# Kernel optimization log

Hardware: AMD Instinct MI355X
Metric: run time of the kernel (lower is better)

## Reference

```python
import jax
jax.config.update("jax_enable_x64", True)
import jax.numpy as jnp
import numpy as np

B = 4            # batch size
Z, Y, X = 41, 1024, 1024   # spatial shape (all coords < 1025, matching the hash base)
NT = 2_000_000   # raw teacher voxels (with duplicates)
NS = 800_000     # student voxels (subset of teacher unique coords)
C = 32           # feature channels
M = 1025         # hash base from the original module


def _hash(idx):
    # idx: [N,4] int -> int64 scalar hash; batch in high bits so sorting the hash
    # == lexicographic sort by (batch, c1, c2, c3), matching torch.unique(dim=0).
    w = jnp.array([M ** 3, M ** 2, M, 1], dtype=jnp.int64)
    return idx.astype(jnp.int64) @ w


def setup_inputs() -> dict:
    rng = np.random.default_rng(0)
    b = rng.integers(0, B, NT)
    z = rng.integers(0, Z, NT)
    y = rng.integers(0, Y, NT)
    x = rng.integers(0, X, NT)
    teacher_indices = np.stack([b, z, y, x], axis=1).astype(np.int32)

    # student indices must be a subset of teacher's unique coords (forward asserts this)
    h = (b.astype(np.int64) * M ** 3 + z.astype(np.int64) * M ** 2
         + y.astype(np.int64) * M + x.astype(np.int64))
    _, first = np.unique(h, return_index=True)
    pick = rng.choice(first, size=NS, replace=False)
    student_indices = teacher_indices[pick]

    key = jax.random.key(0)
    teacher_features = jax.random.normal(key, (NT, C), dtype=jnp.float32)
    return {
        "teacher_features": teacher_features,
        "teacher_indices": jnp.asarray(teacher_indices),
        "student_indices": jnp.asarray(student_indices),
    }


def reference(teacher_features, teacher_indices, student_indices):
    n_t = teacher_indices.shape[0]
    FILL = jnp.int64(2 ** 62)  # padding hash, sorts to the end

    # --- bev_out_3d: unique(dim=0) + index_add_ dedup ---
    h_t = _hash(teacher_indices)
    uniq, first_idx, inv = jnp.unique(
        h_t, size=n_t, fill_value=FILL, return_index=True, return_inverse=True
    )
    feat_unique = jax.ops.segment_sum(teacher_features, inv, num_segments=n_t)

    # --- per-batch isin join + masked gather ---
    # Teacher unique rows are hash-sorted (== lex-sorted by batch, coords).
    # The matched subset, in teacher order, is exactly the sorted student hashes
    # (student is a subset of teacher unique), concatenated batch-by-batch ==
    # a single global sort since batch occupies the high bits.
    h_s = jnp.sort(_hash(student_indices))
    pos = jnp.searchsorted(uniq, h_s)          # [NS] positions into unique rows
    feat = feat_unique[pos]                    # [NS, C]
    indice = teacher_indices[first_idx[pos]]   # [NS, 4]
    return feat, indice
```

## Files before the change

kernel.cpp:

```cpp
#include <hip/hip_runtime.h>
#include <stdint.h>

typedef unsigned long long u64;

#define NWORDS 2686976u
#define GW 4096u
#define NGROUPS 656u

__device__ __forceinline__ uint32_t pack4(int4 v) {
    return (((uint32_t)v.x * 41u + (uint32_t)v.y) << 20) |
           ((uint32_t)v.z << 10) | (uint32_t)v.w;
}

__global__ void set_bits(const int* __restrict__ sidx, u64* __restrict__ words, int ns) {
    int i = blockIdx.x * blockDim.x + threadIdx.x;
    if (i >= ns) return;
    uint32_t k = pack4(((const int4*)sidx)[i]);
    atomicOr(&words[k >> 6], 1ull << (k & 63u));
}

__global__ void group_popcount(const u64* __restrict__ words, uint32_t* __restrict__ groupSum) {
    __shared__ uint32_t s[256];
    uint32_t t = 0;
    size_t base = (size_t)blockIdx.x * GW;
    #pragma unroll
    for (int j = 0; j < 16; ++j)
        t += (uint32_t)__popcll(words[base + j * 256u + threadIdx.x]);
    s[threadIdx.x] = t;
    __syncthreads();
    #pragma unroll
    for (int off = 128; off > 0; off >>= 1) {
        if (threadIdx.x < (unsigned)off) s[threadIdx.x] += s[threadIdx.x + off];
        __syncthreads();
    }
    if (threadIdx.x == 0) groupSum[blockIdx.x] = s[0];
}

__global__ void word_prefix_indice(const u64* __restrict__ words,
                                   const uint32_t* __restrict__ groupSum,
                                   uint32_t* __restrict__ prefixArr,
                                   float* __restrict__ outI) {
    __shared__ uint32_t s[256];
    __shared__ uint32_t baseSh;
    const int tid = threadIdx.x, bid = blockIdx.x;
    size_t w0 = (size_t)bid * GW + (size_t)tid * 16;
    u64 w[16];
    uint32_t tsum = 0;
    #pragma unroll
    for (int j = 0; j < 16; ++j) { w[j] = words[w0 + j]; tsum += (uint32_t)__popcll(w[j]); }
    s[tid] = tsum;
    __syncthreads();
    #pragma unroll
    for (int off = 1; off < 256; off <<= 1) {
        uint32_t u = (tid >= off) ? s[tid - off] : 0u;
        __syncthreads();
        s[tid] += u;
        __syncthreads();
    }
    uint32_t exclInBlock = s[tid] - tsum;
    if (tid < 64) {
        uint32_t sum = 0;
        for (int g = tid; g < bid; g += 64) sum += groupSum[g];
        #pragma unroll
        for (int off = 32; off > 0; off >>= 1) sum += __shfl_down(sum, off);
        if (tid == 0) baseSh = sum;
    }
    __syncthreads();
    uint32_t run = baseSh + exclInBlock;
    #pragma unroll
    for (int j = 0; j < 16; ++j) {
        prefixArr[w0 + j] = run;
        u64 word = w[j];
        uint32_t kw = (uint32_t)(w0 + j) << 6;
        while (word) {
            int b = (int)__builtin_ctzll(word);
            word &= word - 1;
            uint32_t k = kw | (uint32_t)b;
            uint32_t bz = k >> 20;
            ((float4*)outI)[run++] = make_float4(
                (float)(bz / 41u), (float)(bz % 41u),
                (float)((k >> 10) & 1023u), (float)(k & 1023u));
        }
    }
}

__global__ void teacher_fused(const int* __restrict__ tidx, const float* __restrict__ tfeat,
                              const u64* __restrict__ words, const uint32_t* __restrict__ prefixArr,
                              uint32_t* __restrict__ cnt,
                              uint2* __restrict__ ovf, uint32_t* __restrict__ ovfCount,
                              float* __restrict__ feat, int nt) {
    int t = blockIdx.x * blockDim.x + threadIdx.x;
    if (t >= nt) return;
    uint32_t k = pack4(((const int4*)tidx)[t]);
    u64 word = words[k >> 6];
    uint32_t pfx = prefixArr[k >> 6];
    u64 bit = 1ull << (k & 63u);
    if (!(word & bit)) return;
    int p = (int)(pfx + (uint32_t)__popcll(word & (bit - 1ull)));
    const float4* src = (const float4*)(tfeat + (size_t)t * 32);
    float4 f0 = src[0], f1 = src[1], f2 = src[2], f3 = src[3];
    float4 f4 = src[4], f5 = src[5], f6 = src[6], f7 = src[7];
    uint32_t old = atomicAdd(&cnt[p], 1u);
    if (old == 0u) {
        float4* dst = (float4*)(feat + (size_t)p * 32);
        dst[0] = f0; dst[1] = f1; dst[2] = f2; dst[3] = f3;
        dst[4] = f4; dst[5] = f5; dst[6] = f6; dst[7] = f7;
    } else {
        uint32_t idx = atomicAdd(ovfCount, 1u);
        ovf[idx] = make_uint2((uint32_t)t, (uint32_t)p);
    }
}

__global__ void drain_ovf(const float* __restrict__ tfeat, const uint2* __restrict__ ovf,
                          const uint32_t* __restrict__ ovfCount, float* __restrict__ feat) {
    uint32_t n = *ovfCount;
    for (uint32_t i = blockIdx.x * blockDim.x + threadIdx.x; i < n;
         i += gridDim.x * blockDim.x) {
        uint2 e = ovf[i];
        const float4* src = (const float4*)(tfeat + (size_t)e.x * 32);
        float* dst = feat + (size_t)e.y * 32;
        #pragma unroll
        for (int q = 0; q < 8; ++q) {
            float4 f = src[q];
            atomicAdd(dst + q * 4 + 0, f.x);
            atomicAdd(dst + q * 4 + 1, f.y);
            atomicAdd(dst + q * 4 + 2, f.z);
            atomicAdd(dst + q * 4 + 3, f.w);
        }
    }
}

extern "C" void kernel_launch(void* const* d_in, const int* in_sizes, int n_in,
                              void* d_out, int out_size, void* d_ws, size_t ws_size,
                              hipStream_t stream) {
    const float* tfeat = (const float*)d_in[0];
    const int*   tidx  = (const int*)d_in[1];
    const int*   sidx  = (const int*)d_in[2];

    const int NT = in_sizes[1] / 4;
    const int NS = in_sizes[2] / 4;

    float* feat = (float*)d_out;
    float* outI = (float*)d_out + (size_t)NS * 32;

    char* base = (char*)d_ws;
    u64*      words    = (u64*)base;
    uint32_t* cnt      = (uint32_t*)(base + (size_t)NWORDS * 8);
    uint32_t* ovfCount = cnt + NS;
    size_t    zeroBytes = (size_t)NWORDS * 8 + (size_t)NS * 4 + 8;
    uint32_t* groupSum  = ovfCount + 2;
    uint32_t* prefixArr = groupSum + NGROUPS;
    uint2*    ovf       = (uint2*)(prefixArr + NWORDS);

    hipMemsetAsync(d_ws, 0, zeroBytes, stream);

    set_bits<<<(NS + 255) / 256, 256, 0, stream>>>(sidx, words, NS);
    group_popcount<<<NGROUPS, 256, 0, stream>>>(words, groupSum);
    word_prefix_indice<<<NGROUPS, 256, 0, stream>>>(words, groupSum, prefixArr, outI);
    teacher_fused<<<(NT + 255) / 256, 256, 0, stream>>>(tidx, tfeat, words, prefixArr, cnt,
                                                        ovf, ovfCount, feat, NT);
    drain_ovf<<<512, 256, 0, stream>>>(tfeat, ovf, ovfCount, feat);
}
```

Baseline: 212.7 us.

## Split teacher pass into index claim and coalesced row gather kernel

The teacher kernel now only claims an output slot per matched voxel and records the winning teacher row index in an argT array, without loading features. A new gather kernel then copies the 128-byte feature rows using 8 lanes per row, so the writes to the output are coalesced and feature loads for unmatched threads are avoided. This adds a kernel launch, an extra NS-sized zeroed array and an indirection read, and it adds clamping on the overflow count for safety.

```diff
diff --git a/kernel.cpp b/kernel.cpp
--- a/kernel.cpp
+++ b/kernel.cpp
@@ -84,11 +84,10 @@
     }
 }
 
-__global__ void teacher_fused(const int* __restrict__ tidx, const float* __restrict__ tfeat,
+__global__ void teacher_claim(const int* __restrict__ tidx,
                               const u64* __restrict__ words, const uint32_t* __restrict__ prefixArr,
-                              uint32_t* __restrict__ cnt,
-                              uint2* __restrict__ ovf, uint32_t* __restrict__ ovfCount,
-                              float* __restrict__ feat, int nt) {
+                              uint32_t* __restrict__ cnt, int* __restrict__ argT,
+                              uint2* __restrict__ ovf, uint32_t* __restrict__ ovfCount, int nt) {
     int t = blockIdx.x * blockDim.x + threadIdx.x;
     if (t >= nt) return;
     uint32_t k = pack4(((const int4*)tidx)[t]);
@@ -96,24 +95,39 @@
     uint32_t pfx = prefixArr[k >> 6];
     u64 bit = 1ull << (k & 63u);
     if (!(word & bit)) return;
-    int p = (int)(pfx + (uint32_t)__popcll(word & (bit - 1ull)));
-    const float4* src = (const float4*)(tfeat + (size_t)t * 32);
-    float4 f0 = src[0], f1 = src[1], f2 = src[2], f3 = src[3];
-    float4 f4 = src[4], f5 = src[5], f6 = src[6], f7 = src[7];
+    uint32_t p = pfx + (uint32_t)__popcll(word & (bit - 1ull));
     uint32_t old = atomicAdd(&cnt[p], 1u);
     if (old == 0u) {
-        float4* dst = (float4*)(feat + (size_t)p * 32);
-        dst[0] = f0; dst[1] = f1; dst[2] = f2; dst[3] = f3;
-        dst[4] = f4; dst[5] = f5; dst[6] = f6; dst[7] = f7;
+        argT[p] = t;
     } else {
         uint32_t idx = atomicAdd(ovfCount, 1u);
-        ovf[idx] = make_uint2((uint32_t)t, (uint32_t)p);
+        if (idx < (uint32_t)nt) ovf[idx] = make_uint2((uint32_t)t, p);
+    }
+}
+
+__global__ void gather_rows(const float* __restrict__ tfeat, const int* __restrict__ argT,
+                            float* __restrict__ feat, int ns, int nt) {
+    const int tid  = threadIdx.x;
+    const int lane = tid & 63;
+    const int wid  = tid >> 6;
+    const int sub  = lane >> 3;
+    const int fidx = lane & 7;
+    for (int r0 = blockIdx.x * 32; r0 < ns; r0 += gridDim.x * 32) {
+        int r = r0 + wid * 8 + sub;
+        if (r < ns) {
+            uint32_t t = (uint32_t)argT[r];
+            if (t >= (uint32_t)nt) t = 0u;
+            float4 v = ((const float4*)(tfeat + (size_t)t * 32))[fidx];
+            ((float4*)(feat + (size_t)r * 32))[fidx] = v;
+        }
     }
 }
 
 __global__ void drain_ovf(const float* __restrict__ tfeat, const uint2* __restrict__ ovf,
-                          const uint32_t* __restrict__ ovfCount, float* __restrict__ feat) {
+                          const uint32_t* __restrict__ ovfCount, float* __restrict__ feat,
+                          int nt) {
     uint32_t n = *ovfCount;
+    if (n > (uint32_t)nt) n = (uint32_t)nt;
     for (uint32_t i = blockIdx.x * blockDim.x + threadIdx.x; i < n;
          i += gridDim.x * blockDim.x) {
         uint2 e = ovf[i];
@@ -147,8 +161,9 @@
     u64*      words    = (u64*)base;
     uint32_t* cnt      = (uint32_t*)(base + (size_t)NWORDS * 8);
     uint32_t* ovfCount = cnt + NS;
-    size_t    zeroBytes = (size_t)NWORDS * 8 + (size_t)NS * 4 + 8;
-    uint32_t* groupSum  = ovfCount + 2;
+    int*      argT     = (int*)(ovfCount + 2);
+    size_t    zeroBytes = (size_t)NWORDS * 8 + (size_t)NS * 4 + 8 + (size_t)NS * 4;
+    uint32_t* groupSum  = (uint32_t*)(argT + NS);
     uint32_t* prefixArr = groupSum + NGROUPS;
     uint2*    ovf       = (uint2*)(prefixArr + NWORDS);
 
@@ -157,7 +172,8 @@
     set_bits<<<(NS + 255) / 256, 256, 0, stream>>>(sidx, words, NS);
     group_popcount<<<NGROUPS, 256, 0, stream>>>(words, groupSum);
     word_prefix_indice<<<NGROUPS, 256, 0, stream>>>(words, groupSum, prefixArr, outI);
-    teacher_fused<<<(NT + 255) / 256, 256, 0, stream>>>(tidx, tfeat, words, prefixArr, cnt,
-                                                        ovf, ovfCount, feat, NT);
-    drain_ovf<<<512, 256, 0, stream>>>(tfeat, ovf, ovfCount, feat);
+    teacher_claim<<<(NT + 255) / 256, 256, 0, stream>>>(tidx, words, prefixArr, cnt,
+                                                        argT, ovf, ovfCount, NT);
+    gather_rows<<<4096, 256, 0, stream>>>(tfeat, argT, feat, NS, NT);
+    drain_ovf<<<512, 256, 0, stream>>>(tfeat, ovf, ovfCount, feat, NT);
 }
```

New measurement: 217.4 us. 2.2% more time.
